# Optimization experiments

Hardware: AMD Instinct MI355X
Metric: run time of the kernel (lower is better)

## Reference

```python
import jax, jax.numpy as jnp
import numpy as np

NUM_HEADS = 6
NUM_TOKENS = 16
GROUP_SIZE = 32
PRO_COF = 0.4
CENTER_COF = 0.4


def _ln(x, g, b):
    m = jnp.mean(x, axis=-1, keepdims=True)
    v = jnp.var(x, axis=-1, keepdims=True)
    return (x - m) * jax.lax.rsqrt(v + 1e-5) * g + b


def _gelu(x):
    return jax.nn.gelu(x, approximate=False)


def _mhsa(x, qkv_w, proj_w, proj_b, mask=None):
    B, N, C = x.shape
    H = NUM_HEADS
    hd = C // H
    qkv = (x @ qkv_w.T).reshape(B, N, 3, H, hd).transpose(2, 0, 3, 1, 4)
    q, k, v = qkv[0], qkv[1], qkv[2]
    attn = jnp.einsum('bhnd,bhmd->bhnm', q, k) * (hd ** -0.5)
    if mask is not None:
        attn = attn + (mask * -100000.0)[:, None]  # additive mask, broadcast over heads
    attn = jax.nn.softmax(attn, axis=-1)
    out = jnp.einsum('bhnm,bhmd->bhnd', attn, v).transpose(0, 2, 1, 3).reshape(B, N, C)
    return out @ proj_w.T + proj_b


def _adapter(x, dw, db, uw, ub):
    # AdapterSuper: down-proj -> GELU -> up-proj + residual
    return _gelu(x @ dw.T + db) @ uw.T + ub + x


def _forward(x, mask, center1, center2, neighborhood, prompt_embeddings,
             n1_g, n1_b, qkv_w, proj_w, proj_b, n2_g, n2_b,
             fc1_w, fc1_b, fc2_w, fc2_b, ad_gate,
             ad_dw, ad_db, ad_uw, ad_ub, ad1_dw, ad1_db, ad1_uw, ad1_ub,
             bn_g, bn_b, a1_qkv_w, a1_proj_w, a1_proj_b, n3_g, n3_b,
             idx, center_idx):
    B, G1, C = x.shape
    T = NUM_TOKENS
    S = center2.shape[1]
    # mask_new: original mask in top-left, zeros for prompt slots
    mask = jnp.pad(mask, ((0, 0), (0, T), (0, T)))
    prompt = jnp.broadcast_to(prompt_embeddings[None], (B, T, C))
    x = jnp.concatenate([prompt, x], axis=1)                        # [B, T+G1, C]
    x = x + _mhsa(_ln(x, n1_g, n1_b), qkv_w, proj_w, proj_b, mask)
    h = _ln(x, n2_g, n2_b)
    x_fn = _gelu(h @ fc1_w.T + fc1_b) @ fc2_w.T + fc2_b             # MLP (drop_path=0 -> identity)
    x = ad_gate * _adapter(x_fn, ad_dw, ad_db, ad_uw, ad_ub) + x
    prompt = x[:, :T]
    xg = x[:, T:]
    prompt_x = jnp.concatenate([prompt, xg], axis=1)
    flat = prompt_x.reshape(B * (T + G1), C)
    x_neigh = flat[idx].reshape(B * S, GROUP_SIZE, C)               # irregular gather
    x_cent = flat[center_idx].reshape(B, S, C)
    # (neighborhood is normalized by its std in the original but never used afterwards)
    x_neigh = _mhsa(_ln(x_neigh, n3_g, n3_b), a1_qkv_w, a1_proj_w, a1_proj_b) + x_neigh
    knn = x_neigh.reshape(B, S, GROUP_SIZE, C)
    lc = jnp.max(knn, axis=2) + jnp.mean(knn, axis=2)               # if_maxmean=True pooling
    # eval-mode BatchNorm1d with running_mean=0, running_var=1, then GELU
    lc = _gelu(lc * bn_g * jax.lax.rsqrt(jnp.float32(1.0 + 1e-5)) + bn_b)
    vis_x = lc + CENTER_COF * x_cent                                # [B, S, C]
    # propagate: de_neighbors == S, so the sort is a no-op permutation and the
    # inverse-square-distance weighted sum runs over all centers.
    d = (jnp.sum(center1 ** 2, -1)[:, :, None] + jnp.sum(center2 ** 2, -1)[:, None, :]
         - 2.0 * jnp.einsum('bnc,bsc->bns', center1, center2))      # square_distance [B,G1,S]
    recip = 1.0 / (d + 1e-8)
    weight = recip / jnp.sum(recip, axis=-1, keepdims=True)
    interp = jnp.einsum('bns,bsc->bnc', weight, vis_x)
    new_x = xg + PRO_COF * interp
    x = jnp.concatenate([prompt, new_x], axis=1)
    x = _adapter(x, ad1_dw, ad1_db, ad1_uw, ad1_ub)
    return x[:, T:]


def setup_inputs() -> dict:
    key = jax.random.key(0)
    ks = iter(jax.random.split(key, 64))
    B, G, S, T, C, K = 32, 512, 128, NUM_TOKENS, 384, GROUP_SIZE
    H4, R = 4 * C, 16
    f32 = jnp.float32

    def rn(shape, s=0.02):
        return jax.random.normal(next(ks), shape, dtype=f32) * s

    return {
        'x': jax.random.normal(next(ks), (B, G, C), dtype=f32),
        'mask': (jax.random.uniform(next(ks), (B, G, G)) < 0.1).astype(f32),
        'center1': jax.random.normal(next(ks), (B, G, 3), dtype=f32),
        'center2': jax.random.normal(next(ks), (B, S, 3), dtype=f32),
        'neighborhood': jax.random.normal(next(ks), (B, S, K, 3), dtype=f32),
        'prompt_embeddings': rn((T, C)),
        'n1_g': jnp.ones((C,), f32), 'n1_b': jnp.zeros((C,), f32),
        'qkv_w': rn((3 * C, C)), 'proj_w': rn((C, C)), 'proj_b': jnp.zeros((C,), f32),
        'n2_g': jnp.ones((C,), f32), 'n2_b': jnp.zeros((C,), f32),
        'fc1_w': rn((H4, C)), 'fc1_b': jnp.zeros((H4,), f32),
        'fc2_w': rn((C, H4)), 'fc2_b': jnp.zeros((C,), f32),
        'ad_gate': jnp.full((1,), 0.5, f32),
        'ad_dw': rn((R, C)), 'ad_db': jnp.zeros((R,), f32),
        'ad_uw': rn((C, R)), 'ad_ub': jnp.zeros((C,), f32),
        'ad1_dw': rn((R, C)), 'ad1_db': jnp.zeros((R,), f32),
        'ad1_uw': rn((C, R)), 'ad1_ub': jnp.zeros((C,), f32),
        'bn_g': jnp.ones((C,), f32), 'bn_b': jnp.zeros((C,), f32),
        'a1_qkv_w': rn((3 * C, C)), 'a1_proj_w': rn((C, C)), 'a1_proj_b': jnp.zeros((C,), f32),
        'n3_g': jnp.ones((C,), f32), 'n3_b': jnp.zeros((C,), f32),
        'idx': jax.random.randint(next(ks), (B * S * K,), 0, B * (T + G)),
        'center_idx': jax.random.randint(next(ks), (B * S,), 0, B * (T + G)),
    }


def reference(x, mask, center1, center2, neighborhood, prompt_embeddings,
              n1_g, n1_b, qkv_w, proj_w, proj_b, n2_g, n2_b,
              fc1_w, fc1_b, fc2_w, fc2_b, ad_gate,
              ad_dw, ad_db, ad_uw, ad_ub, ad1_dw, ad1_db, ad1_uw, ad1_ub,
              bn_g, bn_b, a1_qkv_w, a1_proj_w, a1_proj_b, n3_g, n3_b,
              idx, center_idx):
    return _forward(x, mask, center1, center2, neighborhood, prompt_embeddings,
                    n1_g, n1_b, qkv_w, proj_w, proj_b, n2_g, n2_b,
                    fc1_w, fc1_b, fc2_w, fc2_b, ad_gate,
                    ad_dw, ad_db, ad_uw, ad_ub, ad1_dw, ad1_db, ad1_uw, ad1_ub,
                    bn_g, bn_b, a1_qkv_w, a1_proj_w, a1_proj_b, n3_g, n3_b,
                    idx, center_idx)
```

## Files before the change

### kernel.cpp

```cpp
#include <hip/hip_runtime.h>
#include <hip/hip_bf16.h>

#define Bq 32
#define Tq 16
#define Gq 512
#define NSEQ 528
#define Cq 384
#define Hq 6
#define Sq 128
#define Kg 32
#define ROWS (Bq*NSEQ)
#define LROWS (Bq*Sq*Kg)

typedef unsigned short u16;
typedef short bf16x8 __attribute__((ext_vector_type(8)));
typedef float f32x4  __attribute__((ext_vector_type(4)));

__device__ __forceinline__ float gelu_f(float x){
    return 0.5f * x * (1.0f + erff(x * 0.70710678118654752f));
}
__device__ __forceinline__ u16 f2b(float x){
    union { float f; unsigned u; } v; v.f = x;
    return (u16)((v.u + 0x7fffu + ((v.u >> 16) & 1u)) >> 16);
}
__device__ __forceinline__ float b2f(u16 h){
    union { float f; unsigned u; } v; v.u = ((unsigned)h) << 16; return v.f;
}

__device__ __forceinline__ void gload16(const u16* g, u16* l){
    __builtin_amdgcn_global_load_lds(
        (const __attribute__((address_space(1))) unsigned int*)(g),
        (__attribute__((address_space(3))) unsigned int*)(l), 16, 0, 0);
}

__global__ void __launch_bounds__(256) prep(const float* __restrict__ qkvw,
    const float* __restrict__ projw, const float* __restrict__ fc1w,
    const float* __restrict__ fc2w, const float* __restrict__ a1qkvw,
    const float* __restrict__ a1pw, u16* __restrict__ WB,
    const float* __restrict__ mask, u16* __restrict__ bias16,
    const float* __restrict__ xin, const float* __restrict__ pe,
    const float* __restrict__ gw, const float* __restrict__ bw,
    float* __restrict__ X, u16* __restrict__ out)
{
    int bid = blockIdx.x;
    if (bid < 9216){
        long i = (long)bid*256 + threadIdx.x;
        if (i >= 2359296) return;
        float v;
        if      (i <  442368) v = qkvw[i];
        else if (i <  589824) v = projw[i -  442368];
        else if (i < 1179648) v = fc1w[i -  589824];
        else if (i < 1769472) v = fc2w[i - 1179648];
        else if (i < 2211840) v = a1qkvw[i - 1769472];
        else                  v = a1pw[i - 2211840];
        WB[i] = f2b(v);
        return;
    }
    if (bid < 17408){
        long i = (long)(bid - 9216)*256 + threadIdx.x;
        if (i >= ((long)Bq*Gq*Gq >> 2)) return;
        float4 v = *(const float4*)(mask + i*4);
        ushort4 r;
        r.x = f2b(-100000.0f * v.x);
        r.y = f2b(-100000.0f * v.y);
        r.z = f2b(-100000.0f * v.z);
        r.w = f2b(-100000.0f * v.w);
        *(ushort4*)(bias16 + i*4) = r;
        return;
    }
    {
        int w = threadIdx.x >> 6, lane = threadIdx.x & 63;
        int row = (bid - 17408)*4 + w;
        if (row >= ROWS) return;
        int p = row % NSEQ; int b = row / NSEQ;
        const float* src = (p < Tq) ? (pe + (long)p*Cq)
                                    : (xin + ((long)b*Gq + (p - Tq))*Cq);
        float v[6]; float s = 0.f, s2 = 0.f;
#pragma unroll
        for (int j = 0; j < 6; j++){ float x = src[lane + 64*j]; v[j] = x; s += x; s2 += x*x; }
#pragma unroll
        for (int m = 1; m < 64; m <<= 1){ s += __shfl_xor(s, m); s2 += __shfl_xor(s2, m); }
        float mean = s * (1.f/384.f);
        float var  = s2 * (1.f/384.f) - mean*mean;
        float rs   = rsqrtf(var + 1e-5f);
        float* xrow = X + (long)row*Cq;
        u16* orow = out + (long)row*Cq;
#pragma unroll
        for (int j = 0; j < 6; j++){
            int c = lane + 64*j;
            xrow[c] = v[j];
            orow[c] = f2b((v[j] - mean) * rs * gw[c] + bw[c]);
        }
    }
}

__global__ void __launch_bounds__(256) ln_rows(const float* __restrict__ in,
    const float* __restrict__ gw, const float* __restrict__ bw,
    u16* __restrict__ out, int rows)
{
    int w = threadIdx.x >> 6, lane = threadIdx.x & 63;
    int row = blockIdx.x*4 + w;
    if (row >= rows) return;
    const float* xr = in + (long)row*Cq;
    float v[6]; float s = 0.f, s2 = 0.f;
#pragma unroll
    for (int j = 0; j < 6; j++){ float x = xr[lane + 64*j]; v[j] = x; s += x; s2 += x*x; }
#pragma unroll
    for (int m = 1; m < 64; m <<= 1){ s += __shfl_xor(s, m); s2 += __shfl_xor(s2, m); }
    float mean = s * (1.f/384.f);
    float var  = s2 * (1.f/384.f) - mean*mean;
    float rs   = rsqrtf(var + 1e-5f);
    u16* orow = out + (long)row*Cq;
#pragma unroll
    for (int j = 0; j < 6; j++){
        int c = lane + 64*j;
        orow[c] = f2b((v[j] - mean) * rs * gw[c] + bw[c]);
    }
}

__global__ void __launch_bounds__(512, 4) gemm_bf16(const u16* __restrict__ A,
    const u16* __restrict__ W, const float* __restrict__ bias,
    float* __restrict__ Cf, u16* __restrict__ Cb, int M, int N, int K, int epi)
{
    __shared__ u16 As0[128*32];
    __shared__ u16 As1[128*32];
    __shared__ u16 Ws0[128*32];
    __shared__ u16 Ws1[128*32];
    int t = threadIdx.x;
    int nx = gridDim.x;
    int nwg = nx * gridDim.y;
    int f = blockIdx.y*nx + blockIdx.x;
    int xcd = f & 7, i = f >> 3;
    int q = nwg >> 3, r = nwg & 7;
    int base = (xcd < r) ? xcd*(q+1) : r*(q+1) + (xcd - r)*q;
    int nf = base + i;
    int m0 = (nf / nx)*128, n0 = (nf % nx)*128;
    int wv = t >> 6, lane = t & 63;
    int wm = (wv >> 2)*64, wn = (wv & 3)*32;
    int fm = lane & 15;
    int fkp = (((lane >> 4) ^ ((fm >> 1) & 3)) & 3) * 8;
    int rs  = t >> 2;
    int kc8 = (((lane & 3) ^ ((lane >> 3) & 3))) * 8;
    f32x4 acc[4][2];
#pragma unroll
    for (int ii = 0; ii < 4; ii++)
#pragma unroll
        for (int j = 0; j < 2; j++) acc[ii][j] = (f32x4){0.f,0.f,0.f,0.f};

    auto STG = [&](u16* Ab, u16* Wb, int k0){
        gload16(A + (long)(m0 + rs)*K + k0 + kc8, Ab + wv*512);
        gload16(W + (long)(n0 + rs)*K + k0 + kc8, Wb + wv*512);
    };
    auto CMP = [&](const u16* Ab, const u16* Wb){
        bf16x8 af[4], bf[2];
#pragma unroll
        for (int im = 0; im < 4; im++) af[im] = *(const bf16x8*)&Ab[(wm + im*16 + fm)*32 + fkp];
#pragma unroll
        for (int in = 0; in < 2; in++) bf[in] = *(const bf16x8*)&Wb[(wn + in*16 + fm)*32 + fkp];
#pragma unroll
        for (int im = 0; im < 4; im++)
#pragma unroll
            for (int in = 0; in < 2; in++)
                acc[im][in] = __builtin_amdgcn_mfma_f32_16x16x32_bf16(af[im], bf[in], acc[im][in], 0, 0, 0);
    };

    int nt = K >> 5;
    STG(As0, Ws0, 0);
    __syncthreads();
    for (int kt = 0; kt < nt; kt += 2){
        STG(As1, Ws1, (kt+1)*32);
        CMP(As0, Ws0);
        __syncthreads();
        if (kt + 2 < nt) STG(As0, Ws0, (kt+2)*32);
        CMP(As1, Ws1);
        __syncthreads();
    }

    int lr = lane >> 4, lc = lane & 15;
#pragma unroll
    for (int im = 0; im < 4; im++){
#pragma unroll
        for (int in = 0; in < 2; in++){
#pragma unroll
            for (int r2 = 0; r2 < 4; r2++){
                int m = m0 + wm + im*16 + lr*4 + r2;
                int n = n0 + wn + in*16 + lc;
                float v = acc[im][in][r2];
                if (epi >= 1 && bias) v += bias[n];
                if (epi == 2) v = gelu_f(v);
                long off = (long)m*N + n;
                if (epi == 3) v += Cf[off];
                if (epi == 2 || epi == 4) Cb[off] = f2b(v);
                else                      Cf[off] = v;
            }
        }
    }
}

__global__ void __launch_bounds__(512, 4) gemm_pool(const u16* __restrict__ A,
    const u16* __restrict__ W, const float* __restrict__ bias,
    const int* __restrict__ idx, const int* __restrict__ cidx,
    const u16* __restrict__ X16, const float* __restrict__ bng,
    const float* __restrict__ bnb, float* __restrict__ vis, int K)
{
    __shared__ u16 As0[128*32];
    __shared__ u16 As1[128*32];
    __shared__ u16 Ws0[128*32];
    __shared__ u16 Ws1[128*32];
    __shared__ int idxl[128];
    __shared__ int cidxl[4];
    int t = threadIdx.x;
    int blkf = blockIdx.x;
    int xcd = blkf & 7, slot = blkf >> 3;
    int m0 = (xcd*128 + slot/3)*128;
    int n0 = (slot % 3)*128;
    if (t < 128) idxl[t] = idx[m0 + t];
    if (t < 4)   cidxl[t] = cidx[(m0 >> 5) + t];
    int wv = t >> 6, lane = t & 63;
    int wm = (wv >> 2)*64, wn = (wv & 3)*32;
    int fm = lane & 15;
    int fkp = (((lane >> 4) ^ ((fm >> 1) & 3)) & 3) * 8;
    int rs  = t >> 2;
    int kc8 = (((lane & 3) ^ ((lane >> 3) & 3))) * 8;
    f32x4 acc[4][2];
#pragma unroll
    for (int ii = 0; ii < 4; ii++)
#pragma unroll
        for (int j = 0; j < 2; j++) acc[ii][j] = (f32x4){0.f,0.f,0.f,0.f};

    auto STG = [&](u16* Ab, u16* Wb, int k0){
        gload16(A + (long)(m0 + rs)*K + k0 + kc8, Ab + wv*512);
        gload16(W + (long)(n0 + rs)*K + k0 + kc8, Wb + wv*512);
    };
    auto CMP = [&](const u16* Ab, const u16* Wb){
        bf16x8 af[4], bf[2];
#pragma unroll
        for (int im = 0; im < 4; im++) af[im] = *(const bf16x8*)&Ab[(wm + im*16 + fm)*32 + fkp];
#pragma unroll
        for (int in = 0; in < 2; in++) bf[in] = *(const bf16x8*)&Wb[(wn + in*16 + fm)*32 + fkp];
#pragma unroll
        for (int im = 0; im < 4; im++)
#pragma unroll
            for (int in = 0; in < 2; in++)
                acc[im][in] = __builtin_amdgcn_mfma_f32_16x16x32_bf16(af[im], bf[in], acc[im][in], 0, 0, 0);
    };

    int nt = K >> 5;
    STG(As0, Ws0, 0);
    __syncthreads();
    for (int kt = 0; kt < nt; kt += 2){
        STG(As1, Ws1, (kt+1)*32);
        CMP(As0, Ws0);
        __syncthreads();
        if (kt + 2 < nt) STG(As0, Ws0, (kt+2)*32);
        CMP(As1, Ws1);
        __syncthreads();
    }

    int lr = lane >> 4, lc = lane & 15;
#pragma unroll
    for (int in = 0; in < 2; in++){
        int c = n0 + wn + in*16 + lc;
        float pb = bias[c];
        float bg = bng[c], bb = bnb[c];
#pragma unroll
        for (int gl = 0; gl < 2; gl++){
            float vmax = -3e38f, vsum = 0.f;
#pragma unroll
            for (int i2 = 0; i2 < 2; i2++){
                int im = gl*2 + i2;
#pragma unroll
                for (int r = 0; r < 4; r++){
                    int rl = wm + im*16 + lr*4 + r;
                    float val = acc[im][in][r] + pb + b2f(X16[(long)idxl[rl]*Cq + c]);
                    vmax = fmaxf(vmax, val); vsum += val;
                }
            }
            vmax = fmaxf(vmax, __shfl_xor(vmax, 16)); vsum += __shfl_xor(vsum, 16);
            vmax = fmaxf(vmax, __shfl_xor(vmax, 32)); vsum += __shfl_xor(vsum, 32);
            if (lane < 16){
                int glb = (wm >> 5) + gl;
                float lcv = vmax + vsum*(1.f/32.f);
                float u = gelu_f(lcv*bg*0.9999950000374997f + bb);
                vis[((long)(m0 >> 5) + glb)*Cq + c] =
                    u + 0.4f*b2f(X16[(long)cidxl[glb]*Cq + c]);
            }
        }
    }
}

__global__ void __launch_bounds__(256) attn_mfma(const u16* __restrict__ QKVg,
    const u16* __restrict__ bias16, u16* __restrict__ out)
{
    __shared__ u16 Ks[32*72];
    __shared__ u16 Vt[64*40];
    __shared__ u16 Bs[64*36];
    __shared__ u16 Pb[4][16*40];
    int blk = blockIdx.x;
    int xcd = blk & 7; int r0 = blk >> 3;
    int bb = r0 & 3;  int rr = r0 >> 2;
    int h = rr % 6;   int qt = rr / 6;
    int b = xcd + 8*bb;
    int t = threadIdx.x; int w = t >> 6; int lane = t & 63;
    int fr  = lane & 15;
    int fko = (lane >> 4) * 8;
    int colj = lane & 15;
    int rgrp = (lane >> 4) * 4;
    int qb0 = qt*64;
    int q0 = qb0 + w*16;

    int qr = q0 + fr; int qrc = qr < NSEQ ? qr : NSEQ-1;
    const u16* qbase = QKVg + (long)(b*NSEQ + qrc)*1152 + h*64;
    bf16x8 aq0 = *(const bf16x8*)(qbase + fko);
    bf16x8 aq1 = *(const bf16x8*)(qbase + 32 + fko);

    f32x4 oacc[4];
#pragma unroll
    for (int d = 0; d < 4; d++) oacc[d] = (f32x4){0.f,0.f,0.f,0.f};
    float lsum[4] = {0.f, 0.f, 0.f, 0.f};

    int skey = t >> 3;
    int sd8  = (t & 7) * 8;
    int jswz = skey ^ ((t & 3) << 3);
    int brow = t >> 2;
    int bc8  = (t & 3) * 8;

    bf16x8 kvR = {0,0,0,0,0,0,0,0}, vvR = {0,0,0,0,0,0,0,0};
    uint4  bzR = make_uint4(0u,0u,0u,0u);
    auto LD = [&](int kc){
        int j = kc*32 + skey;
        bf16x8 kv = {0,0,0,0,0,0,0,0};
        bf16x8 vv = {0,0,0,0,0,0,0,0};
        if (j < NSEQ){
            const u16* kb = QKVg + (long)(b*NSEQ + j)*1152 + 384 + h*64 + sd8;
            kv = *(const bf16x8*)kb;
            vv = *(const bf16x8*)(kb + 384);
        }
        int qi = qb0 + brow;
        int jj = kc*32 + bc8;
        uint4 bz = make_uint4(0u,0u,0u,0u);
        if (qi < Gq && jj < Gq)
            bz = *(const uint4*)(bias16 + ((long)b*Gq + qi)*Gq + jj);
        kvR = kv; vvR = vv; bzR = bz;
    };
    LD(0);

    for (int kc = 0; kc < 17; kc++){
        __syncthreads();
        *(bf16x8*)&Ks[skey*72 + sd8] = kvR;
#pragma unroll
        for (int e = 0; e < 8; e++) Vt[(sd8+e)*40 + jswz] = (u16)kvR[e], Vt[(sd8+e)*40 + jswz] = (u16)vvR[e];
        *(uint4*)&Bs[brow*36 + bc8] = bzR;
        if (kc < 16) LD(kc + 1);
        __syncthreads();

        f32x4 s[2];
#pragma unroll
        for (int sub = 0; sub < 2; sub++){
            bf16x8 bk0 = *(const bf16x8*)&Ks[(sub*16 + fr)*72 + fko];
            bf16x8 bk1 = *(const bf16x8*)&Ks[(sub*16 + fr)*72 + 32 + fko];
            f32x4 z = (f32x4){0.f,0.f,0.f,0.f};
            z = __builtin_amdgcn_mfma_f32_16x16x32_bf16(aq0, bk0, z, 0, 0, 0);
            z = __builtin_amdgcn_mfma_f32_16x16x32_bf16(aq1, bk1, z, 0, 0, 0);
            s[sub] = z;
        }
#pragma unroll
        for (int sub = 0; sub < 2; sub++){
#pragma unroll
            for (int r = 0; r < 4; r++){
                int jj = kc*32 + sub*16 + colj;
                float sv = s[sub][r] * 0.125f
                         + b2f(Bs[(w*16 + rgrp + r)*36 + sub*16 + colj]);
                if (jj >= NSEQ) sv = -1e30f;
                float e = __expf(sv);
                lsum[r] += e;
                Pb[w][(rgrp + r)*40 + sub*16 + colj] = f2b(e);
            }
        }
        bf16x8 ap = *(const bf16x8*)&Pb[w][fr*40 + fko];
#pragma unroll
        for (int d = 0; d < 4; d++){
            int D = d*16 + fr;
            int fkv = fko ^ (((D >> 3) & 3) << 3);
            bf16x8 bv = *(const bf16x8*)&Vt[D*40 + fkv];
            oacc[d] = __builtin_amdgcn_mfma_f32_16x16x32_bf16(ap, bv, oacc[d], 0, 0, 0);
        }
    }
#pragma unroll
    for (int r = 0; r < 4; r++){
#pragma unroll
        for (int mm = 1; mm < 16; mm <<= 1) lsum[r] += __shfl_xor(lsum[r], mm);
    }
#pragma unroll
    for (int r = 0; r < 4; r++){
        int qi = q0 + rgrp + r;
        if (qi < NSEQ){
            float inv = 1.0f / lsum[r];
#pragma unroll
            for (int d = 0; d < 4; d++)
                out[((long)(b*NSEQ + qi))*Cq + h*64 + d*16 + colj] = f2b(oacc[d][r]*inv);
        }
    }
}

__global__ void __launch_bounds__(256) adapter_fused(const float* __restrict__ xfn,
    const float* __restrict__ resid,
    const float* __restrict__ dw, const float* __restrict__ db,
    const float* __restrict__ uw, const float* __restrict__ ub,
    const float* __restrict__ gatep,
    const float* __restrict__ lng, const float* __restrict__ lnb,
    float* __restrict__ Xout, u16* __restrict__ x16out,
    u16* __restrict__ ln16, int rows)
{
    int w = threadIdx.x >> 6, lane = threadIdx.x & 63;
    int row = blockIdx.x*4 + w;
    if (row >= rows) return;
    const float* xr = xfn + (long)row*Cq;
    float xv[6];
#pragma unroll
    for (int j = 0; j < 6; j++) xv[j] = xr[lane + 64*j];
    float hid[16];
#pragma unroll
    for (int r = 0; r < 16; r++){
        const float* dr = dw + r*Cq;
        float p = 0.f;
#pragma unroll
        for (int j = 0; j < 6; j++) p += xv[j]*dr[lane + 64*j];
#pragma unroll
        for (int mm = 1; mm < 64; mm <<= 1) p += __shfl_xor(p, mm);
        hid[r] = gelu_f(p + db[r]);
    }
    float gate = gatep ? gatep[0] : 1.0f;
    float ov[6];
    float s = 0.f, s2 = 0.f;
#pragma unroll
    for (int j = 0; j < 6; j++){
        int c = lane + 64*j;
        const float* uc = uw + c*16;
        float a = 0.f;
#pragma unroll
        for (int r = 0; r < 16; r++) a += hid[r]*uc[r];
        float v = gate * (a + ub[c] + xv[j]);
        if (resid) v += resid[(long)row*Cq + c];
        ov[j] = v;
        Xout[(long)row*Cq + c] = v;
        if (x16out) x16out[(long)row*Cq + c] = f2b(v);
        s += v; s2 += v*v;
    }
    if (lng){
#pragma unroll
        for (int m = 1; m < 64; m <<= 1){ s += __shfl_xor(s, m); s2 += __shfl_xor(s2, m); }
        float mean = s * (1.f/384.f);
        float var  = s2 * (1.f/384.f) - mean*mean;
        float rs   = rsqrtf(var + 1e-5f);
        u16* orow = ln16 + (long)row*Cq;
#pragma unroll
        for (int j = 0; j < 6; j++){
            int c = lane + 64*j;
            orow[c] = f2b((ov[j] - mean)*rs*lng[c] + lnb[c]);
        }
    }
}

__global__ void __launch_bounds__(256) local_attn(const u16* __restrict__ QKVg,
    const int* __restrict__ idx, u16* __restrict__ aout16)
{
    __shared__ u16 Qs[32*72];
    __shared__ u16 Ksm[32*72];
    __shared__ u16 Vt[64*40];
    __shared__ float sc[32*36];
    __shared__ u16 Pa[32*40];
    __shared__ float linv[32];
    __shared__ int rows[32];
    int g = blockIdx.x;
    int t = threadIdx.x;
    int w = t >> 6, lane = t & 63;
    if (t < 32) rows[t] = idx[g*Kg + t];
    __syncthreads();
    int srow = t & 31;
    int d8   = (t >> 5) * 8;
    int jswz = srow ^ (((t >> 5) & 3) << 3);
    int fr = lane & 15, fko = (lane >> 4)*8;
    int colj = lane & 15, rgrp = (lane >> 4)*4;
    int it = w >> 1, jt = w & 1;
    int smrow = w*8 + (lane >> 3);
    int smc   = (lane & 7) * 4;

    const u16* rbase = QKVg + (long)rows[srow]*1152 + d8;
    bf16x8 qvR = *(const bf16x8*)(rbase);
    bf16x8 kvR = *(const bf16x8*)(rbase + 384);
    bf16x8 vvR = *(const bf16x8*)(rbase + 768);

    for (int h = 0; h < Hq; h++){
        *(bf16x8*)&Qs[srow*72 + d8]  = qvR;
        *(bf16x8*)&Ksm[srow*72 + d8] = kvR;
#pragma unroll
        for (int e = 0; e < 8; e++) Vt[(d8+e)*40 + jswz] = (u16)vvR[e];
        if (h < Hq-1){
            const u16* nb = rbase + (h+1)*64;
            qvR = *(const bf16x8*)(nb);
            kvR = *(const bf16x8*)(nb + 384);
            vvR = *(const bf16x8*)(nb + 768);
        }
        __syncthreads();
        {
            bf16x8 a0 = *(const bf16x8*)&Qs[(it*16+fr)*72 + fko];
            bf16x8 a1 = *(const bf16x8*)&Qs[(it*16+fr)*72 + 32 + fko];
            bf16x8 b0 = *(const bf16x8*)&Ksm[(jt*16+fr)*72 + fko];
            bf16x8 b1 = *(const bf16x8*)&Ksm[(jt*16+fr)*72 + 32 + fko];
            f32x4 z = (f32x4){0.f,0.f,0.f,0.f};
            z = __builtin_amdgcn_mfma_f32_16x16x32_bf16(a0, b0, z, 0, 0, 0);
            z = __builtin_amdgcn_mfma_f32_16x16x32_bf16(a1, b1, z, 0, 0, 0);
#pragma unroll
            for (int r = 0; r < 4; r++)
                sc[(it*16 + rgrp + r)*36 + jt*16 + colj] = z[r]*0.125f;
        }
        __syncthreads();
        {
            float4 s4 = *(const float4*)&sc[smrow*36 + smc];
            float mx = fmaxf(fmaxf(s4.x, s4.y), fmaxf(s4.z, s4.w));
#pragma unroll
            for (int mm = 1; mm < 8; mm <<= 1) mx = fmaxf(mx, __shfl_xor(mx, mm));
            float p0 = __expf(s4.x - mx), p1 = __expf(s4.y - mx);
            float p2 = __expf(s4.z - mx), p3 = __expf(s4.w - mx);
            float sm = p0 + p1 + p2 + p3;
#pragma unroll
            for (int mm = 1; mm < 8; mm <<= 1) sm += __shfl_xor(sm, mm);
            if ((lane & 7) == 0) linv[smrow] = 1.0f / sm;
            Pa[smrow*40 + smc + 0] = f2b(p0);
            Pa[smrow*40 + smc + 1] = f2b(p1);
            Pa[smrow*40 + smc + 2] = f2b(p2);
            Pa[smrow*40 + smc + 3] = f2b(p3);
        }
        __syncthreads();
        {
            bf16x8 ap = *(const bf16x8*)&Pa[(it*16+fr)*40 + fko];
#pragma unroll
            for (int dd = 0; dd < 2; dd++){
                int dt = jt + dd*2;
                int D = dt*16 + fr;
                int fkv = fko ^ (((D >> 3) & 3) << 3);
                bf16x8 bv = *(const bf16x8*)&Vt[D*40 + fkv];
                f32x4 o = (f32x4){0.f,0.f,0.f,0.f};
                o = __builtin_amdgcn_mfma_f32_16x16x32_bf16(ap, bv, o, 0, 0, 0);
#pragma unroll
                for (int r = 0; r < 4; r++){
                    int row = it*16 + rgrp + r;
                    aout16[((long)(g*32 + row))*Cq + h*64 + dt*16 + colj] =
                        f2b(o[r] * linv[row]);
                }
            }
        }
        __syncthreads();
    }
}

__global__ void __launch_bounds__(128) interp_k(const float* __restrict__ Xf,
    const float* __restrict__ vis, const float* __restrict__ c1,
    const float* __restrict__ c2, float* __restrict__ newx)
{
    __shared__ float wsh[8*128];
    __shared__ float inv8[8];
    int blk = blockIdx.x;
    int b = blk >> 6, nt = blk & 63;
    int tid = threadIdx.x;
#pragma unroll
    for (int i = 0; i < 8; i++){
        int id = tid + i*128;
        int nl = id >> 7, s = id & 127;
        const float* p1 = c1 + ((long)b*Gq + nt*8 + nl)*3;
        const float* p2 = c2 + ((long)b*Sq + s)*3;
        float x1 = p1[0], y1 = p1[1], z1 = p1[2];
        float x2 = p2[0], y2 = p2[1], z2 = p2[2];
        float d = (x1*x1 + y1*y1 + z1*z1) + (x2*x2 + y2*y2 + z2*z2)
                - 2.f*(x1*x2 + y1*y2 + z1*z2);
        wsh[nl*128 + s] = 1.f/(d + 1e-8f);
    }
    __syncthreads();
    if (tid < 8){
        float sum = 0.f;
        for (int s = 0; s < Sq; s++) sum += wsh[tid*128 + s];
        inv8[tid] = 1.f/sum;
    }
    __syncthreads();
    float acc[8][3];
#pragma unroll
    for (int n = 0; n < 8; n++){ acc[n][0] = 0.f; acc[n][1] = 0.f; acc[n][2] = 0.f; }
    const float* vb = vis + (long)b*Sq*Cq + tid;
    for (int s = 0; s < Sq; s++){
        float v0 = vb[s*Cq], v1 = vb[s*Cq + 128], v2 = vb[s*Cq + 256];
#pragma unroll
        for (int n = 0; n < 8; n++){
            float wq = wsh[n*128 + s];
            acc[n][0] += wq*v0; acc[n][1] += wq*v1; acc[n][2] += wq*v2;
        }
    }
#pragma unroll
    for (int n = 0; n < 8; n++){
        int gn = nt*8 + n;
        const float* xr = Xf + ((long)(b*NSEQ + Tq + gn))*Cq;
        float* orow = newx + ((long)(b*Gq + gn))*Cq;
        float sf = 0.4f * inv8[n];
        orow[tid]       = xr[tid]       + sf*acc[n][0];
        orow[tid + 128] = xr[tid + 128] + sf*acc[n][1];
        orow[tid + 256] = xr[tid + 256] + sf*acc[n][2];
    }
}

extern "C" void kernel_launch(void* const* d_in, const int* in_sizes, int n_in,
                              void* d_out, int out_size, void* d_ws, size_t ws_size,
                              hipStream_t stream)
{
    const float* x_in  = (const float*)d_in[0];
    const float* mask  = (const float*)d_in[1];
    const float* c1p   = (const float*)d_in[2];
    const float* c2p   = (const float*)d_in[3];
    const float* pe    = (const float*)d_in[5];
    const float* n1g   = (const float*)d_in[6];
    const float* n1b   = (const float*)d_in[7];
    const float* qkvw  = (const float*)d_in[8];
    const float* projw = (const float*)d_in[9];
    const float* projb = (const float*)d_in[10];
    const float* n2g   = (const float*)d_in[11];
    const float* n2b   = (const float*)d_in[12];
    const float* fc1w  = (const float*)d_in[13];
    const float* fc1b  = (const float*)d_in[14];
    const float* fc2w  = (const float*)d_in[15];
    const float* fc2b  = (const float*)d_in[16];
    const float* gate  = (const float*)d_in[17];
    const float* addw  = (const float*)d_in[18];
    const float* addb  = (const float*)d_in[19];
    const float* aduw  = (const float*)d_in[20];
    const float* adub  = (const float*)d_in[21];
    const float* ad1dw = (const float*)d_in[22];
    const float* ad1db = (const float*)d_in[23];
    const float* ad1uw = (const float*)d_in[24];
    const float* ad1ub = (const float*)d_in[25];
    const float* bng   = (const float*)d_in[26];
    const float* bnb   = (const float*)d_in[27];
    const float* a1qkvw= (const float*)d_in[28];
    const float* a1pw  = (const float*)d_in[29];
    const float* a1pb  = (const float*)d_in[30];
    const float* n3g   = (const float*)d_in[31];
    const float* n3b   = (const float*)d_in[32];
    const int*   idxp  = (const int*)d_in[33];
    const int*   cidxp = (const int*)d_in[34];

    char* w = (char*)d_ws;
    float* X    = (float*)w;
    u16*   WB   = (u16*)(w + 25952256);
    u16*   Bb16 = (u16*)(w + 30670848);
    char*  R1   = w + 43646976;
    char*  R2   = R1 + 100663296;
    float* V    = (float*)(R2 + 100663296);

    u16* qkvw16  = WB;
    u16* projw16 = WB +  442368;
    u16* fc1w16  = WB +  589824;
    u16* fc2w16  = WB + 1179648;
    u16* a1qkv16 = WB + 1769472;
    u16* a1pw16  = WB + 2211840;

    u16*   bias16 = (u16*)R1;
    u16*   hid16  = (u16*)R1;
    u16*   aout16 = (u16*)R1;
    u16*   QKVg   = (u16*)R2;
    float* C1     = (float*)R2;
    float* newx   = (float*)R2;
    u16*   X16    = (u16*)(R2 + 41943040);

    prep<<<21632, 256, 0, stream>>>(qkvw, projw, fc1w, fc2w, a1qkvw, a1pw, WB,
                                    mask, bias16, x_in, pe, n1g, n1b, X, Bb16);
    gemm_bf16<<<dim3(9, 132), 512, 0, stream>>>(Bb16, qkvw16, nullptr, nullptr, QKVg,
                                                ROWS, 1152, Cq, 4);
    attn_mfma<<<1728, 256, 0, stream>>>(QKVg, bias16, Bb16);
    gemm_bf16<<<dim3(3, 132), 512, 0, stream>>>(Bb16, projw16, projb, X, nullptr,
                                                ROWS, Cq, Cq, 3);
    ln_rows<<<4224, 256, 0, stream>>>(X, n2g, n2b, Bb16, ROWS);
    gemm_bf16<<<dim3(12, 132), 512, 0, stream>>>(Bb16, fc1w16, fc1b, nullptr, hid16,
                                                 ROWS, 1536, Cq, 2);
    gemm_bf16<<<dim3(3, 132), 512, 0, stream>>>(hid16, fc2w16, fc2b, C1, nullptr,
                                                ROWS, Cq, 1536, 1);
    adapter_fused<<<4224, 256, 0, stream>>>(C1, X, addw, addb, aduw, adub, gate,
                                            n3g, n3b, X, X16, Bb16, ROWS);
    gemm_bf16<<<dim3(9, 132), 512, 0, stream>>>(Bb16, a1qkv16, nullptr, nullptr, QKVg,
                                                ROWS, 1152, Cq, 4);
    local_attn<<<4096, 256, 0, stream>>>(QKVg, idxp, aout16);
    gemm_pool<<<3072, 512, 0, stream>>>(aout16, a1pw16, a1pb, idxp, cidxp,
                                        X16, bng, bnb, V, Cq);
    interp_k<<<2048, 128, 0, stream>>>(X, V, c1p, c2p, newx);
    adapter_fused<<<4096, 256, 0, stream>>>(newx, nullptr, ad1dw, ad1db, ad1uw, ad1ub,
                                            nullptr, nullptr, nullptr,
                                            (float*)d_out, nullptr, nullptr, Bq*Gq);
}
```

Before: 683.3 us.

## Load GEMM MFMA fragments directly from global memory, bypassing LDS staging

Measured after the change: 1.139 ms. +66.7%, slower.

```diff
diff --git a/kernel.cpp b/kernel.cpp
--- a/kernel.cpp
+++ b/kernel.cpp
@@ -25,12 +25,6 @@
 }
 __device__ __forceinline__ float b2f(u16 h){
     union { float f; unsigned u; } v; v.u = ((unsigned)h) << 16; return v.f;
-}
-
-__device__ __forceinline__ void gload16(const u16* g, u16* l){
-    __builtin_amdgcn_global_load_lds(
-        (const __attribute__((address_space(1))) unsigned int*)(g),
-        (__attribute__((address_space(3))) unsigned int*)(l), 16, 0, 0);
 }
 
 __global__ void __launch_bounds__(256) prep(const float* __restrict__ qkvw,
@@ -122,10 +116,6 @@
     const u16* __restrict__ W, const float* __restrict__ bias,
     float* __restrict__ Cf, u16* __restrict__ Cb, int M, int N, int K, int epi)
 {
-    __shared__ u16 As0[128*32];
-    __shared__ u16 As1[128*32];
-    __shared__ u16 Ws0[128*32];
-    __shared__ u16 Ws1[128*32];
     int t = threadIdx.x;
     int nx = gridDim.x;
     int nwg = nx * gridDim.y;
@@ -138,25 +128,24 @@
     int wv = t >> 6, lane = t & 63;
     int wm = (wv >> 2)*64, wn = (wv & 3)*32;
     int fm = lane & 15;
-    int fkp = (((lane >> 4) ^ ((fm >> 1) & 3)) & 3) * 8;
-    int rs  = t >> 2;
-    int kc8 = (((lane & 3) ^ ((lane >> 3) & 3))) * 8;
+    int fk = (lane >> 4) * 8;
+    const u16* Abase = A + (long)(m0 + wm + fm)*K + fk;
+    const u16* Wbase = W + (long)(n0 + wn + fm)*K + fk;
     f32x4 acc[4][2];
 #pragma unroll
     for (int ii = 0; ii < 4; ii++)
 #pragma unroll
         for (int j = 0; j < 2; j++) acc[ii][j] = (f32x4){0.f,0.f,0.f,0.f};
 
-    auto STG = [&](u16* Ab, u16* Wb, int k0){
-        gload16(A + (long)(m0 + rs)*K + k0 + kc8, Ab + wv*512);
-        gload16(W + (long)(n0 + rs)*K + k0 + kc8, Wb + wv*512);
+    auto LDF = [&](bf16x8* af, bf16x8* bf, int k0){
+#pragma unroll
+        for (int im = 0; im < 4; im++)
+            af[im] = *(const bf16x8*)(Abase + (long)im*16*K + k0);
+#pragma unroll
+        for (int in = 0; in < 2; in++)
+            bf[in] = *(const bf16x8*)(Wbase + (long)in*16*K + k0);
     };
-    auto CMP = [&](const u16* Ab, const u16* Wb){
-        bf16x8 af[4], bf[2];
-#pragma unroll
-        for (int im = 0; im < 4; im++) af[im] = *(const bf16x8*)&Ab[(wm + im*16 + fm)*32 + fkp];
-#pragma unroll
-        for (int in = 0; in < 2; in++) bf[in] = *(const bf16x8*)&Wb[(wn + in*16 + fm)*32 + fkp];
+    auto CMPF = [&](const bf16x8* af, const bf16x8* bf){
 #pragma unroll
         for (int im = 0; im < 4; im++)
 #pragma unroll
@@ -164,16 +153,13 @@
                 acc[im][in] = __builtin_amdgcn_mfma_f32_16x16x32_bf16(af[im], bf[in], acc[im][in], 0, 0, 0);
     };
 
-    int nt = K >> 5;
-    STG(As0, Ws0, 0);
-    __syncthreads();
-    for (int kt = 0; kt < nt; kt += 2){
-        STG(As1, Ws1, (kt+1)*32);
-        CMP(As0, Ws0);
-        __syncthreads();
-        if (kt + 2 < nt) STG(As0, Ws0, (kt+2)*32);
-        CMP(As1, Ws1);
-        __syncthreads();
+    bf16x8 a0[4], b0[2], a1[4], b1[2];
+    LDF(a0, b0, 0);
+    for (int k0 = 0; k0 < K; k0 += 64){
+        if (k0 + 32 < K) LDF(a1, b1, k0 + 32);
+        CMPF(a0, b0);
+        if (k0 + 64 < K) LDF(a0, b0, k0 + 64);
+        CMPF(a1, b1);
     }
 
     int lr = lane >> 4, lc = lane & 15;
@@ -203,10 +189,6 @@
     const u16* __restrict__ X16, const float* __restrict__ bng,
     const float* __restrict__ bnb, float* __restrict__ vis, int K)
 {
-    __shared__ u16 As0[128*32];
-    __shared__ u16 As1[128*32];
-    __shared__ u16 Ws0[128*32];
-    __shared__ u16 Ws1[128*32];
     __shared__ int idxl[128];
     __shared__ int cidxl[4];
     int t = threadIdx.x;
@@ -219,25 +201,24 @@
     int wv = t >> 6, lane = t & 63;
     int wm = (wv >> 2)*64, wn = (wv & 3)*32;
     int fm = lane & 15;
-    int fkp = (((lane >> 4) ^ ((fm >> 1) & 3)) & 3) * 8;
-    int rs  = t >> 2;
-    int kc8 = (((lane & 3) ^ ((lane >> 3) & 3))) * 8;
+    int fk = (lane >> 4) * 8;
+    const u16* Abase = A + (long)(m0 + wm + fm)*K + fk;
+    const u16* Wbase = W + (long)(n0 + wn + fm)*K + fk;
     f32x4 acc[4][2];
 #pragma unroll
     for (int ii = 0; ii < 4; ii++)
 #pragma unroll
         for (int j = 0; j < 2; j++) acc[ii][j] = (f32x4){0.f,0.f,0.f,0.f};
 
-    auto STG = [&](u16* Ab, u16* Wb, int k0){
-        gload16(A + (long)(m0 + rs)*K + k0 + kc8, Ab + wv*512);
-        gload16(W + (long)(n0 + rs)*K + k0 + kc8, Wb + wv*512);
+    auto LDF = [&](bf16x8* af, bf16x8* bf, int k0){
+#pragma unroll
+        for (int im = 0; im < 4; im++)
+            af[im] = *(const bf16x8*)(Abase + (long)im*16*K + k0);
+#pragma unroll
+        for (int in = 0; in < 2; in++)
+            bf[in] = *(const bf16x8*)(Wbase + (long)in*16*K + k0);
     };
-    auto CMP = [&](const u16* Ab, const u16* Wb){
-        bf16x8 af[4], bf[2];
-#pragma unroll
-        for (int im = 0; im < 4; im++) af[im] = *(const bf16x8*)&Ab[(wm + im*16 + fm)*32 + fkp];
-#pragma unroll
-        for (int in = 0; in < 2; in++) bf[in] = *(const bf16x8*)&Wb[(wn + in*16 + fm)*32 + fkp];
+    auto CMPF = [&](const bf16x8* af, const bf16x8* bf){
 #pragma unroll
         for (int im = 0; im < 4; im++)
 #pragma unroll
@@ -245,17 +226,15 @@
                 acc[im][in] = __builtin_amdgcn_mfma_f32_16x16x32_bf16(af[im], bf[in], acc[im][in], 0, 0, 0);
     };
 
-    int nt = K >> 5;
-    STG(As0, Ws0, 0);
+    bf16x8 a0[4], b0[2], a1[4], b1[2];
+    LDF(a0, b0, 0);
+    for (int k0 = 0; k0 < K; k0 += 64){
+        if (k0 + 32 < K) LDF(a1, b1, k0 + 32);
+        CMPF(a0, b0);
+        if (k0 + 64 < K) LDF(a0, b0, k0 + 64);
+        CMPF(a1, b1);
+    }
     __syncthreads();
-    for (int kt = 0; kt < nt; kt += 2){
-        STG(As1, Ws1, (kt+1)*32);
-        CMP(As0, Ws0);
-        __syncthreads();
-        if (kt + 2 < nt) STG(As0, Ws0, (kt+2)*32);
-        CMP(As1, Ws1);
-        __syncthreads();
-    }
 
     int lr = lane >> 4, lc = lane & 15;
 #pragma unroll
@@ -349,7 +328,7 @@
         __syncthreads();
         *(bf16x8*)&Ks[skey*72 + sd8] = kvR;
 #pragma unroll
-        for (int e = 0; e < 8; e++) Vt[(sd8+e)*40 + jswz] = (u16)kvR[e], Vt[(sd8+e)*40 + jswz] = (u16)vvR[e];
+        for (int e = 0; e < 8; e++) Vt[(sd8+e)*40 + jswz] = (u16)vvR[e];
         *(uint4*)&Bs[brow*36 + bc8] = bzR;
         if (kc < 16) LD(kc + 1);
         __syncthreads();
```

## Pre-pack weights into MFMA fragment layout and use 256-row GEMM tiles

Applied to the files above, without the earlier changes.

Measured after the change: 789.6 us. 1.16x slower.

```diff
diff --git a/kernel.cpp b/kernel.cpp
--- a/kernel.cpp
+++ b/kernel.cpp
@@ -46,14 +46,16 @@
     if (bid < 9216){
         long i = (long)bid*256 + threadIdx.x;
         if (i >= 2359296) return;
-        float v;
-        if      (i <  442368) v = qkvw[i];
-        else if (i <  589824) v = projw[i -  442368];
-        else if (i < 1179648) v = fc1w[i -  589824];
-        else if (i < 1769472) v = fc2w[i - 1179648];
-        else if (i < 2211840) v = a1qkvw[i - 1769472];
-        else                  v = a1pw[i - 2211840];
-        WB[i] = f2b(v);
+        const float* src; long li; int Kx; long off;
+        if      (i <  442368){ src = qkvw;   li = i;           Kx = 384;  off = 0; }
+        else if (i <  589824){ src = projw;  li = i -  442368; Kx = 384;  off =  442368; }
+        else if (i < 1179648){ src = fc1w;   li = i -  589824; Kx = 384;  off =  589824; }
+        else if (i < 1769472){ src = fc2w;   li = i - 1179648; Kx = 1536; off = 1179648; }
+        else if (i < 2211840){ src = a1qkvw; li = i - 1769472; Kx = 384;  off = 1769472; }
+        else                 { src = a1pw;   li = i - 2211840; Kx = 384;  off = 2211840; }
+        int n = (int)(li / Kx), k = (int)(li % Kx);
+        long d = off + ((long)(n >> 4)*(Kx >> 5) + (k >> 5))*512 + (n & 15)*32 + (k & 31);
+        WB[d] = f2b(src[li]);
         return;
     }
     if (bid < 17408){
@@ -118,14 +120,12 @@
     }
 }
 
-__global__ void __launch_bounds__(512, 4) gemm_bf16(const u16* __restrict__ A,
-    const u16* __restrict__ W, const float* __restrict__ bias,
+__global__ void __launch_bounds__(512, 4) gemm256(const u16* __restrict__ A,
+    const u16* __restrict__ Wp, const float* __restrict__ bias,
     float* __restrict__ Cf, u16* __restrict__ Cb, int M, int N, int K, int epi)
 {
-    __shared__ u16 As0[128*32];
-    __shared__ u16 As1[128*32];
-    __shared__ u16 Ws0[128*32];
-    __shared__ u16 Ws1[128*32];
+    __shared__ u16 As0[256*32];
+    __shared__ u16 As1[256*32];
     int t = threadIdx.x;
     int nx = gridDim.x;
     int nwg = nx * gridDim.y;
@@ -134,45 +134,49 @@
     int q = nwg >> 3, r = nwg & 7;
     int base = (xcd < r) ? xcd*(q+1) : r*(q+1) + (xcd - r)*q;
     int nf = base + i;
-    int m0 = (nf / nx)*128, n0 = (nf % nx)*128;
+    int m0 = (nf / nx)*256, n0 = (nf % nx)*128;
     int wv = t >> 6, lane = t & 63;
-    int wm = (wv >> 2)*64, wn = (wv & 3)*32;
+    int wm = (wv >> 1)*64, wn = (wv & 1)*64;
     int fm = lane & 15;
+    int fk = (lane >> 4) * 8;
     int fkp = (((lane >> 4) ^ ((fm >> 1) & 3)) & 3) * 8;
     int rs  = t >> 2;
     int kc8 = (((lane & 3) ^ ((lane >> 3) & 3))) * 8;
-    f32x4 acc[4][2];
+    const u16* Wbase = Wp + (long)((n0 + wn) >> 4)*K*16 + fm*32 + fk;
+    f32x4 acc[4][4];
 #pragma unroll
     for (int ii = 0; ii < 4; ii++)
 #pragma unroll
-        for (int j = 0; j < 2; j++) acc[ii][j] = (f32x4){0.f,0.f,0.f,0.f};
-
-    auto STG = [&](u16* Ab, u16* Wb, int k0){
+        for (int j = 0; j < 4; j++) acc[ii][j] = (f32x4){0.f,0.f,0.f,0.f};
+
+    auto STG = [&](u16* Ab, int k0){
         gload16(A + (long)(m0 + rs)*K + k0 + kc8, Ab + wv*512);
-        gload16(W + (long)(n0 + rs)*K + k0 + kc8, Wb + wv*512);
+        gload16(A + (long)(m0 + 128 + rs)*K + k0 + kc8, Ab + 4096 + wv*512);
     };
-    auto CMP = [&](const u16* Ab, const u16* Wb){
-        bf16x8 af[4], bf[2];
-#pragma unroll
-        for (int im = 0; im < 4; im++) af[im] = *(const bf16x8*)&Ab[(wm + im*16 + fm)*32 + fkp];
-#pragma unroll
-        for (int in = 0; in < 2; in++) bf[in] = *(const bf16x8*)&Wb[(wn + in*16 + fm)*32 + fkp];
+    auto CMP = [&](const u16* Ab, int k0){
+        bf16x8 af[4], bf[4];
+#pragma unroll
+        for (int in = 0; in < 4; in++)
+            bf[in] = *(const bf16x8*)(Wbase + (long)in*K*16 + k0*16);
 #pragma unroll
         for (int im = 0; im < 4; im++)
-#pragma unroll
-            for (int in = 0; in < 2; in++)
+            af[im] = *(const bf16x8*)&Ab[(wm + im*16 + fm)*32 + fkp];
+#pragma unroll
+        for (int im = 0; im < 4; im++)
+#pragma unroll
+            for (int in = 0; in < 4; in++)
                 acc[im][in] = __builtin_amdgcn_mfma_f32_16x16x32_bf16(af[im], bf[in], acc[im][in], 0, 0, 0);
     };
 
     int nt = K >> 5;
-    STG(As0, Ws0, 0);
+    STG(As0, 0);
     __syncthreads();
     for (int kt = 0; kt < nt; kt += 2){
-        STG(As1, Ws1, (kt+1)*32);
-        CMP(As0, Ws0);
-        __syncthreads();
-        if (kt + 2 < nt) STG(As0, Ws0, (kt+2)*32);
-        CMP(As1, Ws1);
+        STG(As1, (kt+1)*32);
+        CMP(As0, kt*32);
+        __syncthreads();
+        if (kt + 2 < nt) STG(As0, (kt+2)*32);
+        CMP(As1, (kt+1)*32);
         __syncthreads();
     }
 
@@ -180,7 +184,7 @@
 #pragma unroll
     for (int im = 0; im < 4; im++){
 #pragma unroll
-        for (int in = 0; in < 2; in++){
+        for (int in = 0; in < 4; in++){
 #pragma unroll
             for (int r2 = 0; r2 < 4; r2++){
                 int m = m0 + wm + im*16 + lr*4 + r2;
@@ -198,68 +202,70 @@
 }
 
 __global__ void __launch_bounds__(512, 4) gemm_pool(const u16* __restrict__ A,
-    const u16* __restrict__ W, const float* __restrict__ bias,
+    const u16* __restrict__ Wp, const float* __restrict__ bias,
     const int* __restrict__ idx, const int* __restrict__ cidx,
     const u16* __restrict__ X16, const float* __restrict__ bng,
     const float* __restrict__ bnb, float* __restrict__ vis, int K)
 {
-    __shared__ u16 As0[128*32];
-    __shared__ u16 As1[128*32];
-    __shared__ u16 Ws0[128*32];
-    __shared__ u16 Ws1[128*32];
-    __shared__ int idxl[128];
-    __shared__ int cidxl[4];
+    __shared__ u16 As0[256*32];
+    __shared__ u16 As1[256*32];
+    __shared__ int idxl[256];
+    __shared__ int cidxl[8];
     int t = threadIdx.x;
     int blkf = blockIdx.x;
     int xcd = blkf & 7, slot = blkf >> 3;
-    int m0 = (xcd*128 + slot/3)*128;
+    int m0 = (xcd*64 + slot/3)*256;
     int n0 = (slot % 3)*128;
-    if (t < 128) idxl[t] = idx[m0 + t];
-    if (t < 4)   cidxl[t] = cidx[(m0 >> 5) + t];
+    if (t < 256) idxl[t] = idx[m0 + t];
+    if (t < 8)   cidxl[t] = cidx[(m0 >> 5) + t];
     int wv = t >> 6, lane = t & 63;
-    int wm = (wv >> 2)*64, wn = (wv & 3)*32;
+    int wm = (wv >> 1)*64, wn = (wv & 1)*64;
     int fm = lane & 15;
+    int fk = (lane >> 4) * 8;
     int fkp = (((lane >> 4) ^ ((fm >> 1) & 3)) & 3) * 8;
     int rs  = t >> 2;
     int kc8 = (((lane & 3) ^ ((lane >> 3) & 3))) * 8;
-    f32x4 acc[4][2];
+    const u16* Wbase = Wp + (long)((n0 + wn) >> 4)*K*16 + fm*32 + fk;
+    f32x4 acc[4][4];
 #pragma unroll
     for (int ii = 0; ii < 4; ii++)
 #pragma unroll
-        for (int j = 0; j < 2; j++) acc[ii][j] = (f32x4){0.f,0.f,0.f,0.f};
-
-    auto STG = [&](u16* Ab, u16* Wb, int k0){
+        for (int j = 0; j < 4; j++) acc[ii][j] = (f32x4){0.f,0.f,0.f,0.f};
+
+    auto STG = [&](u16* Ab, int k0){
         gload16(A + (long)(m0 + rs)*K + k0 + kc8, Ab + wv*512);
-        gload16(W + (long)(n0 + rs)*K + k0 + kc8, Wb + wv*512);
+        gload16(A + (long)(m0 + 128 + rs)*K + k0 + kc8, Ab + 4096 + wv*512);
     };
-    auto CMP = [&](const u16* Ab, const u16* Wb){
-        bf16x8 af[4], bf[2];
-#pragma unroll
-        for (int im = 0; im < 4; im++) af[im] = *(const bf16x8*)&Ab[(wm + im*16 + fm)*32 + fkp];
-#pragma unroll
-        for (int in = 0; in < 2; in++) bf[in] = *(const bf16x8*)&Wb[(wn + in*16 + fm)*32 + fkp];
+    auto CMP = [&](const u16* Ab, int k0){
+        bf16x8 af[4], bf[4];
+#pragma unroll
+        for (int in = 0; in < 4; in++)
+            bf[in] = *(const bf16x8*)(Wbase + (long)in*K*16 + k0*16);
 #pragma unroll
         for (int im = 0; im < 4; im++)
-#pragma unroll
-            for (int in = 0; in < 2; in++)
+            af[im] = *(const bf16x8*)&Ab[(wm + im*16 + fm)*32 + fkp];
+#pragma unroll
+        for (int im = 0; im < 4; im++)
+#pragma unroll
+            for (int in = 0; in < 4; in++)
                 acc[im][in] = __builtin_amdgcn_mfma_f32_16x16x32_bf16(af[im], bf[in], acc[im][in], 0, 0, 0);
     };
 
     int nt = K >> 5;
-    STG(As0, Ws0, 0);
+    STG(As0, 0);
     __syncthreads();
     for (int kt = 0; kt < nt; kt += 2){
-        STG(As1, Ws1, (kt+1)*32);
-        CMP(As0, Ws0);
-        __syncthreads();
-        if (kt + 2 < nt) STG(As0, Ws0, (kt+2)*32);
-        CMP(As1, Ws1);
+        STG(As1, (kt+1)*32);
+        CMP(As0, kt*32);
+        __syncthreads();
+        if (kt + 2 < nt) STG(As0, (kt+2)*32);
+        CMP(As1, (kt+1)*32);
         __syncthreads();
     }
 
     int lr = lane >> 4, lc = lane & 15;
 #pragma unroll
-    for (int in = 0; in < 2; in++){
+    for (int in = 0; in < 4; in++){
         int c = n0 + wn + in*16 + lc;
         float pb = bias[c];
         float bg = bng[c], bb = bnb[c];
@@ -349,7 +355,7 @@
         __syncthreads();
         *(bf16x8*)&Ks[skey*72 + sd8] = kvR;
 #pragma unroll
-        for (int e = 0; e < 8; e++) Vt[(sd8+e)*40 + jswz] = (u16)kvR[e], Vt[(sd8+e)*40 + jswz] = (u16)vvR[e];
+        for (int e = 0; e < 8; e++) Vt[(sd8+e)*40 + jswz] = (u16)vvR[e];
         *(uint4*)&Bs[brow*36 + bc8] = bzR;
         if (kc < 16) LD(kc + 1);
         __syncthreads();
@@ -671,22 +677,22 @@
 
     prep<<<21632, 256, 0, stream>>>(qkvw, projw, fc1w, fc2w, a1qkvw, a1pw, WB,
                                     mask, bias16, x_in, pe, n1g, n1b, X, Bb16);
-    gemm_bf16<<<dim3(9, 132), 512, 0, stream>>>(Bb16, qkvw16, nullptr, nullptr, QKVg,
-                                                ROWS, 1152, Cq, 4);
+    gemm256<<<dim3(9, 66), 512, 0, stream>>>(Bb16, qkvw16, nullptr, nullptr, QKVg,
+                                             ROWS, 1152, Cq, 4);
     attn_mfma<<<1728, 256, 0, stream>>>(QKVg, bias16, Bb16);
-    gemm_bf16<<<dim3(3, 132), 512, 0, stream>>>(Bb16, projw16, projb, X, nullptr,
-                                                ROWS, Cq, Cq, 3);
+    gemm256<<<dim3(3, 66), 512, 0, stream>>>(Bb16, projw16, projb, X, nullptr,
+                                             ROWS, Cq, Cq, 3);
     ln_rows<<<4224, 256, 0, stream>>>(X, n2g, n2b, Bb16, ROWS);
-    gemm_bf16<<<dim3(12, 132), 512, 0, stream>>>(Bb16, fc1w16, fc1b, nullptr, hid16,
-                                                 ROWS, 1536, Cq, 2);
-    gemm_bf16<<<dim3(3, 132), 512, 0, stream>>>(hid16, fc2w16, fc2b, C1, nullptr,
-                                                ROWS, Cq, 1536, 1);
+    gemm256<<<dim3(12, 66), 512, 0, stream>>>(Bb16, fc1w16, fc1b, nullptr, hid16,
+                                              ROWS, 1536, Cq, 2);
+    gemm256<<<dim3(3, 66), 512, 0, stream>>>(hid16, fc2w16, fc2b, C1, nullptr,
+                                             ROWS, Cq, 1536, 1);
     adapter_fused<<<4224, 256, 0, stream>>>(C1, X, addw, addb, aduw, adub, gate,
                                             n3g, n3b, X, X16, Bb16, ROWS);
-    gemm_bf16<<<dim3(9, 132), 512, 0, stream>>>(Bb16, a1qkv16, nullptr, nullptr, QKVg,
-                                                ROWS, 1152, Cq, 4);
+    gemm256<<<dim3(9, 66), 512, 0, stream>>>(Bb16, a1qkv16, nullptr, nullptr, QKVg,
+                                             ROWS, 1152, Cq, 4);
     local_attn<<<4096, 256, 0, stream>>>(QKVg, idxp, aout16);
-    gemm_pool<<<3072, 512, 0, stream>>>(aout16, a1pw16, a1pb, idxp, cidxp,
+    gemm_pool<<<1536, 512, 0, stream>>>(aout16, a1pw16, a1pb, idxp, cidxp,
                                         X16, bng, bnb, V, Cq);
     interp_k<<<2048, 128, 0, stream>>>(X, V, c1p, c2p, newx);
     adapter_fused<<<4096, 256, 0, stream>>>(newx, nullptr, ad1dw, ad1db, ad1uw, ad1ub,
```
